# Performance work log

Measured on AMD Instinct MI355X. Metric: run time of the kernel, lower is better.

The kernel has to match this reference:

```python
import jax, jax.numpy as jnp
import numpy as np

B, S, D_IN, D_H = 8, 2048, 512, 512

def setup_inputs() -> dict:
    key = jax.random.key(0)
    ks = jax.random.split(key, 7)
    s = 1.0 / np.sqrt(D_IN)
    return {
        "x": jax.random.normal(ks[0], (B, S, D_IN), dtype=jnp.float32),
        "Wq": jax.random.uniform(ks[1], (D_H, D_IN), jnp.float32, -s, s),
        "bq": jax.random.uniform(ks[2], (D_H,), jnp.float32, -s, s),
        "Wk": jax.random.uniform(ks[3], (D_H, D_IN), jnp.float32, -s, s),
        "bk": jax.random.uniform(ks[4], (D_H,), jnp.float32, -s, s),
        "Wv": jax.random.uniform(ks[5], (D_H, D_IN), jnp.float32, -s, s),
        "bv": jax.random.uniform(ks[6], (D_H,), jnp.float32, -s, s),
    }

def reference(x, Wq, bq, Wk, bk, Wv, bv):
    # torch Linear: y = x @ W.T + b
    Q = jnp.einsum('bsd,hd->bsh', x, Wq) + bq
    K = jnp.einsum('bsd,hd->bsh', x, Wk) + bk
    V = jnp.einsum('bsd,hd->bsh', x, Wv) + bv
    scale = jnp.sqrt(jnp.asarray(D_H, dtype=x.dtype))
    scores = jnp.einsum('bqh,bkh->bqk', Q, K) / scale  # [B,S,S]
    attn = jax.nn.softmax(scores, axis=-1)
    return jnp.einsum('bqk,bkh->bqh', attn, V)
```

## Files before the change

kernel.cpp:

```cpp
#include <hip/hip_runtime.h>
#include <hip/hip_bf16.h>
#include <cstdint>

#define B_   8
#define S_   2048
#define DIN  512
#define DH   512

typedef __attribute__((ext_vector_type(8))) short  short8;
typedef __attribute__((ext_vector_type(4))) short  short4_;
typedef __attribute__((ext_vector_type(4))) float  float4_;

__device__ inline unsigned short f2bf(float f) {
    union { float f; unsigned u; } v; v.f = f;
    unsigned u = v.u;
    u += 0x7fffu + ((u >> 16) & 1u);
    return (unsigned short)(u >> 16);
}

__device__ inline void gload_lds16(const void* g, void* l) {
    __builtin_amdgcn_global_load_lds(
        (const __attribute__((address_space(1))) void*)g,
        (__attribute__((address_space(3))) void*)l, 16, 0, 0);
}

template <int C>
__device__ inline float fdpp(float x) {
    return __int_as_float(__builtin_amdgcn_update_dpp(0, __float_as_int(x), C, 0xF, 0xF, true));
}
__device__ inline float rsum16(float v) {
    v += fdpp<0x140>(v);
    v += fdpp<0x141>(v);
    v += fdpp<27>(v);
    v += fdpp<177>(v);
    return v;
}

__global__ __launch_bounds__(256) void conv_bf16(
    const float* __restrict__ x,
    const float* __restrict__ Wq, const float* __restrict__ Wk, const float* __restrict__ Wv,
    unsigned short* __restrict__ xb, unsigned short* __restrict__ wb)
{
    const int NX4 = (B_ * S_ * DIN) / 4;
    const int NW4 = (DH * DIN) / 4;
    const int total = NX4 + 3 * NW4;
    for (int i = blockIdx.x * blockDim.x + threadIdx.x; i < total;
         i += gridDim.x * blockDim.x) {
        const float4_* src; unsigned short* dst; int j;
        if (i < NX4)             { src = (const float4_*)x;  dst = xb;            j = i; }
        else if (i < NX4 + NW4)  { src = (const float4_*)Wq; dst = wb;            j = i - NX4; }
        else if (i < NX4 + 2*NW4){ src = (const float4_*)Wk; dst = wb + DH*DIN;   j = i - NX4 - NW4; }
        else                     { src = (const float4_*)Wv; dst = wb + 2*DH*DIN; j = i - NX4 - 2*NW4; }
        float4_ v = src[j];
        short4_ o;
        o[0] = (short)f2bf(v[0]); o[1] = (short)f2bf(v[1]);
        o[2] = (short)f2bf(v[2]); o[3] = (short)f2bf(v[3]);
        ((short4_*)dst)[j] = o;
    }
}

__global__ __launch_bounds__(256) void qkv_gemm(
    const unsigned short* __restrict__ xb,
    const unsigned short* __restrict__ wb,
    const float* __restrict__ bq, const float* __restrict__ bk, const float* __restrict__ bv,
    unsigned short* __restrict__ qws, unsigned short* __restrict__ kws,
    unsigned short* __restrict__ vt2)
{
    __shared__ __align__(16) unsigned short smem[17408];

    const int tm   = blockIdx.x;
    const int tc   = blockIdx.y;
    const int mat  = tc >> 2;
    const int nb   = (tc & 3) * 128;
    const int tid  = threadIdx.x;
    const int w    = tid >> 6;
    const int lane = tid & 63;
    const int l15  = lane & 15;
    const int quad = lane >> 4;
    const int wm   = (w & 1) * 64;
    const int wn   = (w >> 1) * 64;
    const int m0   = tm * 128;

    const unsigned short* wmat = wb + (size_t)mat * DH * DIN;

    float4_ zero = {0.f, 0.f, 0.f, 0.f};
    float4_ acc[4][4];
    #pragma unroll
    for (int i = 0; i < 4; i++)
        #pragma unroll
        for (int j = 0; j < 4; j++) acc[i][j] = zero;

    const int lr = lane >> 2;
    const int lb = (lane & 3) * 16;

    auto stage = [&](int kk, int bufi) {
        unsigned short* Ab = smem + bufi * 8192;
        unsigned short* Bb = smem + 4096 + bufi * 8192;
        #pragma unroll
        for (int c = 0; c < 2; c++) {
            int r = w * 32 + c * 16;
            const unsigned char* gA = (const unsigned char*)(xb + (size_t)(m0 + r) * DIN + kk);
            gload_lds16(gA + (size_t)lr * (DIN * 2) + lb, (void*)(Ab + r * 32));
            const unsigned char* gB = (const unsigned char*)(wmat + (size_t)(nb + r) * DIN + kk);
            gload_lds16(gB + (size_t)lr * (DIN * 2) + lb, (void*)(Bb + r * 32));
        }
    };

    stage(0, 0);
    for (int ki = 0; ki < 16; ki++) {
        __syncthreads();
        if (ki < 15) stage((ki + 1) * 32, (ki + 1) & 1);
        const unsigned short* Ab = smem + (ki & 1) * 8192;
        const unsigned short* Bb = smem + 4096 + (ki & 1) * 8192;
        short8 af[4], bf[4];
        #pragma unroll
        for (int mt = 0; mt < 4; mt++)
            af[mt] = *(const short8*)(Ab + (wm + mt * 16 + l15) * 32 + quad * 8);
        #pragma unroll
        for (int nt = 0; nt < 4; nt++)
            bf[nt] = *(const short8*)(Bb + (wn + nt * 16 + l15) * 32 + quad * 8);
        #pragma unroll
        for (int mt = 0; mt < 4; mt++)
            #pragma unroll
            for (int nt = 0; nt < 4; nt++)
                acc[mt][nt] = __builtin_amdgcn_mfma_f32_16x16x32_bf16(af[mt], bf[nt], acc[mt][nt], 0, 0, 0);
    }

    if (mat < 2) {
        const float* bias  = (mat == 0) ? bq : bk;
        const float  scale = (mat == 0) ? 0.06375870430742225f : 1.0f;
        unsigned short* dst = (mat == 0) ? qws : kws;
        #pragma unroll
        for (int nt = 0; nt < 4; nt++) {
            int n = nb + wn + nt * 16 + l15;
            float bv_ = bias[n];
            #pragma unroll
            for (int mt = 0; mt < 4; mt++) {
                #pragma unroll
                for (int r = 0; r < 4; r++) {
                    int m = m0 + wm + mt * 16 + quad * 4 + r;
                    dst[(size_t)m * DH + n] = f2bf((acc[mt][nt][r] + bv_) * scale);
                }
            }
        }
    } else {
        __syncthreads();
        unsigned short* trans = smem;
        #pragma unroll
        for (int nt = 0; nt < 4; nt++) {
            int dloc = wn + nt * 16 + l15;
            float bv_ = bv[nb + dloc];
            #pragma unroll
            for (int mt = 0; mt < 4; mt++) {
                short4_ pk;
                #pragma unroll
                for (int r = 0; r < 4; r++) pk[r] = (short)f2bf(acc[mt][nt][r] + bv_);
                *(short4_*)(trans + dloc * 136 + wm + mt * 16 + quad * 4) = pk;
            }
        }
        __syncthreads();
        int dl   = tid >> 1;
        int h    = tid & 1;
        int dh_g = nb + dl;
        int bi   = m0 >> 11;
        int tile0 = (m0 & 2047) >> 4;
        unsigned char* vt2b = (unsigned char*)vt2;
        #pragma unroll
        for (int t = 0; t < 4; t++) {
            int tl = h * 4 + t;
            const uint4* c = (const uint4*)(trans + dl * 136 + tl * 16);
            unsigned char* dst = vt2b + ((size_t)(bi * 128 + tile0 + tl) << 14) + dh_g * 32;
            ((uint4*)dst)[0] = c[0];
            ((uint4*)dst)[1] = c[1];
        }
    }
}

__global__ __launch_bounds__(512, 2) void attn(
    const unsigned short* __restrict__ qws,
    const unsigned short* __restrict__ kws,
    const unsigned short* __restrict__ vt2,
    float* __restrict__ out)
{
    __shared__ __align__(16) unsigned char smem[76288];

    const int bid  = blockIdx.x;
    const int b    = bid & 7;
    const int qt_b = bid >> 3;
    const int tid  = threadIdx.x;
    const int w    = tid >> 6;
    const int g    = w >> 2;
    const int wl   = w & 3;
    const int lane = tid & 63;
    const int l15  = lane & 15;
    const int quad = lane >> 4;

    const int qrow0  = b * S_ + qt_b * 64;
    const int myqrow = qrow0 + wl * 16;

    const unsigned short* kgrp = kws + (size_t)(b * S_ + g * 1024) * DH;
    const unsigned char*  vtb  = (const unsigned char*)vt2;

    unsigned char* kb    = smem + g * 32768;
    unsigned char* pbase = smem + 65536 + g * 5120;
    float*         lbuf  = (float*)(smem + 75776);

    short8 qf[16];
    {
        const short8* qp = (const short8*)(qws + (size_t)(myqrow + l15) * DH);
        #pragma unroll
        for (int ksi = 0; ksi < 16; ksi++) qf[ksi] = qp[ksi * 4 + quad];
    }

    float4_ zero = {0.f, 0.f, 0.f, 0.f};
    float4_ o[16];
    #pragma unroll
    for (int i = 0; i < 16; i++) o[i] = zero;
    float l_[4] = {0.f, 0.f, 0.f, 0.f};

    short8 vreg[4];

    auto stageK = [&](int n, int bufi) {
        #pragma unroll
        for (int i = 0; i < 4; i++) {
            int row = wl * 4 + i;
            const unsigned char* gp =
                (const unsigned char*)(kgrp + (size_t)(n * 16 + row) * DH);
            gload_lds16(gp + ((lane ^ (row & 7)) << 4),
                        kb + bufi * 16384 + row * 1024);
        }
    };

    auto loadV = [&](int n) {
        const unsigned char* base = vtb
            + ((size_t)(b * 128 + (quad >> 1) * 64 + n) << 14) + (quad & 1) * 16;
        #pragma unroll
        for (int dht = 0; dht < 4; dht++)
            vreg[dht] = *(const short8*)(base + (size_t)(w * 64 + dht * 16 + l15) * 32);
    };

    auto doPV = [&](int bufi) {
        const unsigned char* pq = smem + 65536 + (quad >> 1) * 5120
                                + bufi * 2560 + (quad & 1) * 16;
        short8 pa[4];
        #pragma unroll
        for (int qt = 0; qt < 4; qt++)
            pa[qt] = *(const short8*)(pq + (qt * 16 + l15) * 40);
        #pragma unroll
        for (int dht = 0; dht < 4; dht++) {
            #pragma unroll
            for (int qt = 0; qt < 4; qt++)
                o[qt * 4 + dht] = __builtin_amdgcn_mfma_f32_16x16x32_bf16(pa[qt], vreg[dht], o[qt * 4 + dht], 0, 0, 0);
        }
    };

    stageK(0, 0);

    for (int it = 0; it < 64; it++) {
        __syncthreads();

        if (it) loadV(it - 1);
        if (it < 63) stageK(it + 1, (it + 1) & 1);

        const unsigned char* kt_ = kb + (it & 1) * 16384;
        float4_ s0 = zero, s1 = zero;
        #pragma unroll
        for (int ksi = 0; ksi < 16; ksi += 2) {
            short8 k0 = *(const short8*)(kt_ + l15 * 1024 + ((( ksi      * 4 + quad) ^ (l15 & 7)) << 4));
            short8 k1 = *(const short8*)(kt_ + l15 * 1024 + ((((ksi + 1) * 4 + quad) ^ (l15 & 7)) << 4));
            s0 = __builtin_amdgcn_mfma_f32_16x16x32_bf16(qf[ksi],     k0, s0, 0, 0, 0);
            s1 = __builtin_amdgcn_mfma_f32_16x16x32_bf16(qf[ksi + 1], k1, s1, 0, 0, 0);
        }
        float4_ sc = s0 + s1;

        unsigned short* pp = (unsigned short*)(pbase + (it & 1) * 2560);
        #pragma unroll
        for (int r = 0; r < 4; r++) {
            float p = __builtin_exp2f(sc[r]);
            l_[r] += p;
            pp[(wl * 16 + quad * 4 + r) * 20 + l15] = f2bf(p);
        }

        if (it) doPV((it - 1) & 1);
    }

    __syncthreads();
    loadV(63);
    doPV(1);

    float lsum[4];
    #pragma unroll
    for (int r = 0; r < 4; r++) lsum[r] = rsum16(l_[r]);
    if (l15 == 0) {
        #pragma unroll
        for (int r = 0; r < 4; r++)
            lbuf[g * 64 + wl * 16 + quad * 4 + r] = lsum[r];
    }
    __syncthreads();

    #pragma unroll
    for (int qt = 0; qt < 4; qt++) {
        float rl[4];
        #pragma unroll
        for (int r = 0; r < 4; r++) {
            int row = qt * 16 + quad * 4 + r;
            rl[r] = 1.f / (lbuf[row] + lbuf[64 + row]);
        }
        #pragma unroll
        for (int dht = 0; dht < 4; dht++)
            #pragma unroll
            for (int r = 0; r < 4; r++) {
                int row = qt * 16 + quad * 4 + r;
                out[(size_t)(qrow0 + row) * DH + w * 64 + dht * 16 + l15] =
                    o[qt * 4 + dht][r] * rl[r];
            }
    }
}

extern "C" void kernel_launch(void* const* d_in, const int* in_sizes, int n_in,
                              void* d_out, int out_size, void* d_ws, size_t ws_size,
                              hipStream_t stream) {
    const float* x  = (const float*)d_in[0];
    const float* Wq = (const float*)d_in[1];
    const float* bq = (const float*)d_in[2];
    const float* Wk = (const float*)d_in[3];
    const float* bk = (const float*)d_in[4];
    const float* Wv = (const float*)d_in[5];
    const float* bv = (const float*)d_in[6];
    float* out = (float*)d_out;

    unsigned short* qws = (unsigned short*)d_ws;
    unsigned short* kws = qws + (size_t)B_ * S_ * DH;
    unsigned short* vt2 = kws + (size_t)B_ * S_ * DH;

    unsigned short* xb = (unsigned short*)d_out;
    unsigned short* wb = xb + (size_t)B_ * S_ * DIN;

    conv_bf16<<<dim3(2048), dim3(256), 0, stream>>>(x, Wq, Wk, Wv, xb, wb);
    qkv_gemm<<<dim3(128, 12), dim3(256), 0, stream>>>(xb, wb, bq, bk, bv, qws, kws, vt2);
    attn<<<dim3(256), dim3(512), 0, stream>>>(qws, kws, vt2, out);
}
```

Measured before the change: 256.8 us.

## Repartition attention blocks to 32 query rows with four key-split groups

The attention kernel now gives each block 32 query rows instead of 64 and launches twice as many blocks. Within a block the eight warps form four key-range groups of two warps each, instead of two groups of four. Each warp keeps fewer output accumulators, loads more V fragments, and covers a 128-wide slice of the head dimension. P is now shared through one larger LDS buffer that spans all four key groups, and the row sums are reduced across four partials. The goal is more parallelism and better CU fill, at the cost of much larger LDS use (about 137KB), which likely allows only one block per CU despite launch_bounds(512,2). It also reloads K and V for twice as many blocks.

```diff
diff --git a/kernel.cpp b/kernel.cpp
--- a/kernel.cpp
+++ b/kernel.cpp
@@ -182,85 +182,85 @@
     const unsigned short* __restrict__ vt2,
     float* __restrict__ out)
 {
-    __shared__ __align__(16) unsigned char smem[76288];
+    __shared__ __align__(16) unsigned char smem[140288];
 
     const int bid  = blockIdx.x;
     const int b    = bid & 7;
-    const int qt_b = bid >> 3;
+    const int qb   = bid >> 3;
     const int tid  = threadIdx.x;
     const int w    = tid >> 6;
-    const int g    = w >> 2;
-    const int wl   = w & 3;
+    const int g    = w >> 1;
+    const int h    = w & 1;
     const int lane = tid & 63;
     const int l15  = lane & 15;
     const int quad = lane >> 4;
 
-    const int qrow0  = b * S_ + qt_b * 64;
-    const int myqrow = qrow0 + wl * 16;
-
-    const unsigned short* kgrp = kws + (size_t)(b * S_ + g * 1024) * DH;
+    const int qrow0 = b * S_ + qb * 32;
+
+    const unsigned short* kgrp = kws + (size_t)(b * S_ + g * 512) * DH;
     const unsigned char*  vtb  = (const unsigned char*)vt2;
 
-    unsigned char* kb    = smem + g * 32768;
-    unsigned char* pbase = smem + 65536 + g * 5120;
-    float*         lbuf  = (float*)(smem + 75776);
+    unsigned char* kb   = smem + g * 32768;
+    float*         lbuf = (float*)(smem + 139776);
 
     short8 qf[16];
     {
-        const short8* qp = (const short8*)(qws + (size_t)(myqrow + l15) * DH);
+        const short8* qp = (const short8*)(qws + (size_t)(qrow0 + h * 16 + l15) * DH);
         #pragma unroll
         for (int ksi = 0; ksi < 16; ksi++) qf[ksi] = qp[ksi * 4 + quad];
     }
 
     float4_ zero = {0.f, 0.f, 0.f, 0.f};
-    float4_ o[16];
+    float4_ o[8];
     #pragma unroll
-    for (int i = 0; i < 16; i++) o[i] = zero;
+    for (int i = 0; i < 8; i++) o[i] = zero;
     float l_[4] = {0.f, 0.f, 0.f, 0.f};
 
-    short8 vreg[4];
-
-    auto stageK = [&](int n, int bufi) {
-        #pragma unroll
-        for (int i = 0; i < 4; i++) {
-            int row = wl * 4 + i;
+    short8 vreg[16];
+
+    auto stageK = [&](int n, int par) {
+        #pragma unroll
+        for (int i = 0; i < 8; i++) {
+            int row = h * 8 + i;
             const unsigned char* gp =
                 (const unsigned char*)(kgrp + (size_t)(n * 16 + row) * DH);
             gload_lds16(gp + ((lane ^ (row & 7)) << 4),
-                        kb + bufi * 16384 + row * 1024);
+                        kb + par * 16384 + row * 1024);
         }
     };
 
     auto loadV = [&](int n) {
-        const unsigned char* base = vtb
-            + ((size_t)(b * 128 + (quad >> 1) * 64 + n) << 14) + (quad & 1) * 16;
-        #pragma unroll
-        for (int dht = 0; dht < 4; dht++)
-            vreg[dht] = *(const short8*)(base + (size_t)(w * 64 + dht * 16 + l15) * 32);
+        const unsigned char* b0 = vtb
+            + ((size_t)(b * 128 + ((quad >> 1)    ) * 32 + n) << 14)
+            + g * 4096 + l15 * 32 + (quad & 1) * 16;
+        const unsigned char* b1 = vtb
+            + ((size_t)(b * 128 + (2 + (quad >> 1)) * 32 + n) << 14)
+            + g * 4096 + l15 * 32 + (quad & 1) * 16;
+        #pragma unroll
+        for (int dht = 0; dht < 8; dht++) {
+            vreg[dht * 2 + 0] = *(const short8*)(b0 + dht * 512);
+            vreg[dht * 2 + 1] = *(const short8*)(b1 + dht * 512);
+        }
     };
 
-    auto doPV = [&](int bufi) {
-        const unsigned char* pq = smem + 65536 + (quad >> 1) * 5120
-                                + bufi * 2560 + (quad & 1) * 16;
-        short8 pa[4];
-        #pragma unroll
-        for (int qt = 0; qt < 4; qt++)
-            pa[qt] = *(const short8*)(pq + (qt * 16 + l15) * 40);
-        #pragma unroll
-        for (int dht = 0; dht < 4; dht++) {
-            #pragma unroll
-            for (int qt = 0; qt < 4; qt++)
-                o[qt * 4 + dht] = __builtin_amdgcn_mfma_f32_16x16x32_bf16(pa[qt], vreg[dht], o[qt * 4 + dht], 0, 0, 0);
+    auto doPV = [&](int par) {
+        const unsigned char* pb = smem + 131072 + par * 4352 + (h * 16 + l15) * 136 + quad * 16;
+        short8 pa0 = *(const short8*)(pb);
+        short8 pa1 = *(const short8*)(pb + 64);
+        #pragma unroll
+        for (int dht = 0; dht < 8; dht++) {
+            o[dht] = __builtin_amdgcn_mfma_f32_16x16x32_bf16(pa0, vreg[dht * 2 + 0], o[dht], 0, 0, 0);
+            o[dht] = __builtin_amdgcn_mfma_f32_16x16x32_bf16(pa1, vreg[dht * 2 + 1], o[dht], 0, 0, 0);
         }
     };
 
     stageK(0, 0);
 
-    for (int it = 0; it < 64; it++) {
+    for (int it = 0; it < 32; it++) {
         __syncthreads();
 
         if (it) loadV(it - 1);
-        if (it < 63) stageK(it + 1, (it + 1) & 1);
+        if (it < 31) stageK(it + 1, (it + 1) & 1);
 
         const unsigned char* kt_ = kb + (it & 1) * 16384;
         float4_ s0 = zero, s1 = zero;
@@ -273,47 +273,41 @@
         }
         float4_ sc = s0 + s1;
 
-        unsigned short* pp = (unsigned short*)(pbase + (it & 1) * 2560);
+        unsigned short* pp = (unsigned short*)(smem + 131072 + (it & 1) * 4352);
         #pragma unroll
         for (int r = 0; r < 4; r++) {
             float p = __builtin_exp2f(sc[r]);
             l_[r] += p;
-            pp[(wl * 16 + quad * 4 + r) * 20 + l15] = f2bf(p);
+            pp[(h * 16 + quad * 4 + r) * 68 + g * 16 + l15] = f2bf(p);
         }
 
         if (it) doPV((it - 1) & 1);
     }
 
     __syncthreads();
-    loadV(63);
+    loadV(31);
     doPV(1);
 
-    float lsum[4];
+    {
+        float lsum[4];
+        #pragma unroll
+        for (int r = 0; r < 4; r++) lsum[r] = rsum16(l_[r]);
+        if (l15 == 0) {
+            #pragma unroll
+            for (int r = 0; r < 4; r++)
+                lbuf[g * 32 + h * 16 + quad * 4 + r] = lsum[r];
+        }
+    }
+    __syncthreads();
+
     #pragma unroll
-    for (int r = 0; r < 4; r++) lsum[r] = rsum16(l_[r]);
-    if (l15 == 0) {
-        #pragma unroll
-        for (int r = 0; r < 4; r++)
-            lbuf[g * 64 + wl * 16 + quad * 4 + r] = lsum[r];
-    }
-    __syncthreads();
-
-    #pragma unroll
-    for (int qt = 0; qt < 4; qt++) {
-        float rl[4];
-        #pragma unroll
-        for (int r = 0; r < 4; r++) {
-            int row = qt * 16 + quad * 4 + r;
-            rl[r] = 1.f / (lbuf[row] + lbuf[64 + row]);
-        }
-        #pragma unroll
-        for (int dht = 0; dht < 4; dht++)
-            #pragma unroll
-            for (int r = 0; r < 4; r++) {
-                int row = qt * 16 + quad * 4 + r;
-                out[(size_t)(qrow0 + row) * DH + w * 64 + dht * 16 + l15] =
-                    o[qt * 4 + dht][r] * rl[r];
-            }
+    for (int r = 0; r < 4; r++) {
+        int row = h * 16 + quad * 4 + r;
+        float rl = 1.f / (lbuf[row] + lbuf[32 + row] + lbuf[64 + row] + lbuf[96 + row]);
+        #pragma unroll
+        for (int dht = 0; dht < 8; dht++)
+            out[(size_t)(qrow0 + row) * DH + g * 128 + dht * 16 + l15] =
+                o[dht][r] * rl;
     }
 }
 
@@ -338,5 +332,5 @@
 
     conv_bf16<<<dim3(2048), dim3(256), 0, stream>>>(x, Wq, Wk, Wv, xb, wb);
     qkv_gemm<<<dim3(128, 12), dim3(256), 0, stream>>>(xb, wb, bq, bk, bv, qws, kws, vt2);
-    attn<<<dim3(256), dim3(512), 0, stream>>>(qws, kws, vt2, out);
-}
+    attn<<<dim3(512), dim3(512), 0, stream>>>(qws, kws, vt2, out);
+}
```

New measurement: 370.6 us. 44.3% more time.
